# Optimization experiments

Measured on AMD Instinct MI355X. Metric: run time of the kernel, lower is better.

The kernel has to match this reference:

```python
import jax, jax.numpy as jnp
import numpy as np

E = 1024   # embed_dim
H = 16     # num_heads
D = E // H # head_dim = 64
B = 2
S = 2048

def setup_inputs() -> dict:
    key = jax.random.key(0)
    ks = jax.random.split(key, 11)
    std = 0.02
    return {
        "query": jax.random.normal(ks[0], (B, S, E), jnp.float32),
        "key":   jax.random.normal(ks[1], (B, S, E), jnp.float32),
        "value": jax.random.normal(ks[2], (B, S, E), jnp.float32),
        "Wq": std * jax.random.normal(ks[3], (E, E), jnp.float32),
        "bq": jnp.zeros((E,), jnp.float32),
        "Wk": std * jax.random.normal(ks[4], (D, E), jnp.float32),
        "bk": jnp.zeros((D,), jnp.float32),
        "Wv": std * jax.random.normal(ks[5], (D, E), jnp.float32),
        "bv": jnp.zeros((D,), jnp.float32),
        "Wo": std * jax.random.normal(ks[6], (E, E), jnp.float32),
        "bo": jnp.zeros((E,), jnp.float32),
    }

def reference(query, key, value, Wq, bq, Wk, bk, Wv, bv, Wo, bo):
    b, t, _ = query.shape
    scaling = D ** -0.5
    q = query @ Wq.T + bq                      # [B, T, E]
    k = key @ Wk.T + bk                        # [B, S, D] (single shared KV head)
    v = value @ Wv.T + bv                      # [B, S, D]
    q = q.reshape(b, t, H, D).transpose(0, 2, 1, 3) * scaling  # [B, H, T, D]
    # MQA: broadcast shared k/v across heads inside einsum (no materialized expand)
    attn_weights = jnp.einsum("bhtd,bsd->bhts", q, k)          # [B, H, T, S]
    attn_probs = jax.nn.softmax(attn_weights, axis=-1)
    attn_output = jnp.einsum("bhts,bsd->bhtd", attn_probs, v)  # [B, H, T, D]
    attn_output = attn_output.transpose(0, 2, 1, 3).reshape(b, t, E)
    return attn_output @ Wo.T + bo
```

## Files before the change

kernel.cpp:

```cpp
#include <hip/hip_runtime.h>

#define E_DIM  1024
#define H_HEADS 16
#define D_HEAD  64
#define B_BATCH 2
#define S_SEQ  2048
#define M_ROWS (B_BATCH * S_SEQ)

typedef unsigned short u16;
typedef unsigned int   u32;
typedef __attribute__((ext_vector_type(8))) short bf16x8;
typedef __attribute__((ext_vector_type(4))) short bf16x4;
typedef __attribute__((ext_vector_type(4))) float f32x4;

#define MFMA32(a, b, c) __builtin_amdgcn_mfma_f32_16x16x32_bf16(a, b, c, 0, 0, 0)

#if __has_builtin(__builtin_amdgcn_mfma_f32_16x16x16bf16_1k)
#define HAVE_MFMA16 1
#define MFMA16(a, b, c) __builtin_amdgcn_mfma_f32_16x16x16bf16_1k(a, b, c, 0, 0, 0)
#else
#define HAVE_MFMA16 0
#endif

__device__ __forceinline__ u16 f2bf(float f) {
    union { float f; u32 i; } x; x.f = f;
    u32 r = x.i + 0x7fffu + ((x.i >> 16) & 1u);
    return (u16)(r >> 16);
}

#if __has_builtin(__builtin_amdgcn_cvt_pk_bf16_f32)
typedef __attribute__((ext_vector_type(2))) __bf16 bfp2;
__device__ __forceinline__ u32 pk2(float a, float b) {
    bfp2 t = __builtin_amdgcn_cvt_pk_bf16_f32(a, b);
    union { bfp2 v; u32 u; } c; c.v = t; return c.u;
}
#else
__device__ __forceinline__ u32 pk2(float a, float b) {
    return (u32)f2bf(a) | ((u32)f2bf(b) << 16);
}
#endif

__device__ __forceinline__ bf16x8 cvt8(const float4& a, const float4& b) {
    union { u32 u[4]; bf16x8 v; } t;
    t.u[0] = pk2(a.x, a.y); t.u[1] = pk2(a.z, a.w);
    t.u[2] = pk2(b.x, b.y); t.u[3] = pk2(b.z, b.w);
    return t.v;
}
__device__ __forceinline__ bf16x4 pack4(const f32x4& v) {
    union { u32 u[2]; bf16x4 w; } t;
    t.u[0] = pk2(v[0], v[1]); t.u[1] = pk2(v[2], v[3]);
    return t.w;
}

__device__ __forceinline__ void gl_lds16(const u16* g, u16* l) {
    __builtin_amdgcn_global_load_lds(
        (const __attribute__((address_space(1))) u32*)g,
        (__attribute__((address_space(3))) u32*)l, 16, 0, 0);
}

__global__ __launch_bounds__(256) void cast_all_kernel(
    const float* __restrict__ q,  const float* __restrict__ wq,
    const float* __restrict__ wo,
    u16* __restrict__ qo, u16* __restrict__ wqo, u16* __restrict__ woo)
{
    const int bid = blockIdx.x;
    const float* src; u16* dst; size_t base;
    if (bid < 2048)      { src = q;  dst = qo;  base = (size_t)bid * 2048; }
    else if (bid < 2560) { src = wq; dst = wqo; base = (size_t)(bid - 2048) * 2048; }
    else                 { src = wo; dst = woo; base = (size_t)(bid - 2560) * 2048; }
    const size_t i = base + (size_t)threadIdx.x * 8;
    float4 a = ((const float4*)(src + i))[0];
    float4 b = ((const float4*)(src + i))[1];
    *(bf16x8*)(dst + i) = cvt8(a, b);
}

template<bool OUT_BF16>
__global__ __launch_bounds__(256, 2) void gemm_bf16_kernel(
    const u16* __restrict__ A, const u16* __restrict__ W,
    const float* __restrict__ bias, void* __restrict__ Cv,
    int M, int N, int K, float scale)
{
    __shared__ u16 Asm[2][2][128 * 32];
    __shared__ u16 Bsm[2][2][64 * 32];

    const int tid = threadIdx.x;
    const int w  = tid >> 6;
    const int ln = tid & 63;
    const int n  = ln & 15;
    const int qd = ln >> 4;
    const int wm = (w & 1) * 64;
    const int wn = (w >> 1) * 32;

    const int m0 = blockIdx.y * 128;
    const int n0 = blockIdx.x * 64;

    const int srow = tid >> 2;
    const int sblk = tid & 3;
    const int sc   = (sblk ^ (srow & 3)) * 8;

    f32x4 acc[4][2];
#pragma unroll
    for (int mt = 0; mt < 4; mt++)
#pragma unroll
        for (int nt = 0; nt < 2; nt++) acc[mt][nt] = (f32x4){0.f, 0.f, 0.f, 0.f};

    auto stageA = [&](int p, int k0) {
#pragma unroll
        for (int kb = 0; kb < 2; kb++)
#pragma unroll
            for (int g = 0; g < 2; g++) {
                const int row = g * 64 + srow;
                gl_lds16(A + (size_t)(m0 + row) * K + k0 + kb * 32 + sc,
                         &Asm[p][kb][row * 32 + sblk * 8]);
            }
    };
    auto stageB = [&](int p, int k0) {
#pragma unroll
        for (int kb = 0; kb < 2; kb++)
            gl_lds16(W + (size_t)(n0 + srow) * K + k0 + kb * 32 + sc,
                     &Bsm[p][kb][srow * 32 + sblk * 8]);
    };
    auto compute = [&](int p) {
        bf16x8 af[4][2], bfr[2][2];
#pragma unroll
        for (int kb = 0; kb < 2; kb++) {
#pragma unroll
            for (int mt = 0; mt < 4; mt++) {
                const int r = wm + mt * 16 + n;
                af[mt][kb] = *(const bf16x8*)&Asm[p][kb][r * 32 + ((qd ^ (n & 3)) * 8)];
            }
#pragma unroll
            for (int nt = 0; nt < 2; nt++) {
                const int r = wn + nt * 16 + n;
                bfr[nt][kb] = *(const bf16x8*)&Bsm[p][kb][r * 32 + ((qd ^ (n & 3)) * 8)];
            }
        }
#pragma unroll
        for (int kb = 0; kb < 2; kb++)
#pragma unroll
            for (int mt = 0; mt < 4; mt++)
#pragma unroll
                for (int nt = 0; nt < 2; nt++)
                    acc[mt][nt] = MFMA32(af[mt][kb], bfr[nt][kb], acc[mt][nt]);
    };

    stageA(0, 0); stageB(0, 0);

    int p = 0;
    for (int k0 = 64; k0 < K; k0 += 64) {
        __syncthreads();
        stageA(p ^ 1, k0);
        stageB(p ^ 1, k0);
        compute(p);
        p ^= 1;
    }
    __syncthreads();
    compute(p);

    float bb[2];
#pragma unroll
    for (int nt = 0; nt < 2; nt++) bb[nt] = bias[n0 + wn + nt * 16 + n] * scale;

#pragma unroll
    for (int mt = 0; mt < 4; mt++)
#pragma unroll
        for (int r = 0; r < 4; r++) {
            const int row = m0 + wm + mt * 16 + qd * 4 + r;
#pragma unroll
            for (int nt = 0; nt < 2; nt++) {
                const int col = n0 + wn + nt * 16 + n;
                float v = acc[mt][nt][r] * scale + bb[nt];
                if (OUT_BF16) ((u16*)Cv)[(size_t)row * N + col] = f2bf(v);
                else        ((float*)Cv)[(size_t)row * N + col] = v;
            }
        }
}

__global__ __launch_bounds__(256) void kv_proj_kernel(
    const float* __restrict__ key, const float* __restrict__ value,
    const float* __restrict__ Wk, const float* __restrict__ Wv,
    const float* __restrict__ bk, const float* __restrict__ bv,
    u16* __restrict__ Kout, u16* __restrict__ VTout, int M, int K)
{
    const bool vproj = (blockIdx.y == 1);
    const float* A    = vproj ? value : key;
    const float* W    = vproj ? Wv : Wk;
    const float* bias = vproj ? bv : bk;

    __shared__ u16 Asm[64 * 32];
    __shared__ u16 Bsm[64 * 32];

    const int tid = threadIdx.x;
    const int w  = tid >> 6;
    const int ln = tid & 63;
    const int n  = ln & 15;
    const int qd = ln >> 4;
    const int wm = (w & 1) * 32;
    const int wn = (w >> 1) * 32;
    const int m0 = blockIdx.x * 64;

    const int srow = tid >> 2;
    const int scol = (tid & 3) * 8;

    f32x4 acc[2][2];
#pragma unroll
    for (int mt = 0; mt < 2; mt++)
#pragma unroll
        for (int nt = 0; nt < 2; nt++) acc[mt][nt] = (f32x4){0.f, 0.f, 0.f, 0.f};

    for (int k0 = 0; k0 < K; k0 += 32) {
        __syncthreads();
        const float* pa = A + (size_t)(m0 + srow) * K + k0 + scol;
        const float* pw = W + (size_t)srow * K + k0 + scol;
        float4 a0 = ((const float4*)pa)[0], a1 = ((const float4*)pa)[1];
        float4 w0 = ((const float4*)pw)[0], w1 = ((const float4*)pw)[1];
        *(bf16x8*)&Asm[srow * 32 + scol] = cvt8(a0, a1);
        *(bf16x8*)&Bsm[srow * 32 + scol] = cvt8(w0, w1);
        __syncthreads();

        bf16x8 af[2], bfr[2];
#pragma unroll
        for (int t = 0; t < 2; t++) {
            af[t]  = *(const bf16x8*)&Asm[(wm + t * 16 + n) * 32 + qd * 8];
            bfr[t] = *(const bf16x8*)&Bsm[(wn + t * 16 + n) * 32 + qd * 8];
        }
#pragma unroll
        for (int mt = 0; mt < 2; mt++)
#pragma unroll
            for (int nt = 0; nt < 2; nt++)
                acc[mt][nt] = MFMA32(af[mt], bfr[nt], acc[mt][nt]);
    }

    if (!vproj) {
#pragma unroll
        for (int mt = 0; mt < 2; mt++)
#pragma unroll
            for (int r = 0; r < 4; r++) {
                const int row = m0 + wm + mt * 16 + qd * 4 + r;
#pragma unroll
                for (int nt = 0; nt < 2; nt++) {
                    const int col = wn + nt * 16 + n;
                    Kout[(size_t)row * 64 + col] = f2bf(acc[mt][nt][r] + bias[col]);
                }
            }
    } else {
#pragma unroll
        for (int mt = 0; mt < 2; mt++)
#pragma unroll
            for (int nt = 0; nt < 2; nt++) {
                const int col = wn + nt * 16 + n;
                const int row0 = m0 + wm + mt * 16 + qd * 4;
                float b4 = bias[col];
                ushort4 pk;
                pk.x = f2bf(acc[mt][nt][0] + b4);
                pk.y = f2bf(acc[mt][nt][1] + b4);
                pk.z = f2bf(acc[mt][nt][2] + b4);
                pk.w = f2bf(acc[mt][nt][3] + b4);
                *(ushort4*)&VTout[(size_t)col * M + row0] = pk;
            }
    }
}

__global__ __launch_bounds__(256, 3) void mqa_attn_mfma_kernel(
    const u16* Q, const u16* __restrict__ K,
    const u16* __restrict__ VT, u16* O)
{
    __shared__ u16 ksm[2][128 * 32];
    __shared__ u16 vsm[4][64 * 32];
#if !HAVE_MFMA16
    __shared__ u16 psm[4][32 * 128];
#endif

    const int tid = threadIdx.x;
    const int w   = tid >> 6;
    const int ln  = tid & 63;
    const int n   = ln & 15;
    const int qd  = ln >> 4;
    const int lr  = ln >> 2;
    const int blk = ln & 3;
    const int rb  = lr & 3;

    const int bid = blockIdx.x;
    const int qb = bid & 15;
    const int h  = (bid >> 4) & (H_HEADS - 1);
    const int b  = bid >> 8;
    const int q0 = qb * 128;

    {
        const u16* qg = Q + (size_t)(b * S_SEQ + q0) * E_DIM + h * 64;
#pragma unroll
        for (int kb = 0; kb < 2; kb++)
#pragma unroll
            for (int j = 0; j < 2; j++) {
                int row = w * 32 + j * 16 + lr;
                gl_lds16(qg + (size_t)row * E_DIM + kb * 32 + ((blk ^ rb) * 8),
                         &ksm[kb][row * 32 + blk * 8]);
            }
    }
    __syncthreads();

    bf16x8 qa[2][2];
#pragma unroll
    for (int mt = 0; mt < 2; mt++)
#pragma unroll
        for (int kb = 0; kb < 2; kb++) {
            int row = w * 32 + mt * 16 + n;
            qa[mt][kb] = *(const bf16x8*)&ksm[kb][row * 32 + ((qd ^ (n & 3)) * 8)];
        }

    f32x4 acc_o[2][4];
    float lsum[2] = {0.f, 0.f};
#pragma unroll
    for (int mt = 0; mt < 2; mt++)
#pragma unroll
        for (int ntd = 0; ntd < 4; ntd++) acc_o[mt][ntd] = (f32x4){0.f, 0.f, 0.f, 0.f};

    const u16* kg = K  + (size_t)b * S_SEQ * 64;
    const u16* vg = VT + (size_t)b * S_SEQ;

    for (int s0 = 0; s0 < S_SEQ; s0 += 128) {
        __syncthreads();
#pragma unroll
        for (int kb = 0; kb < 2; kb++)
#pragma unroll
            for (int j = 0; j < 2; j++) {
                int row = w * 32 + j * 16 + lr;
                gl_lds16(kg + (size_t)(s0 + row) * 64 + kb * 32 + ((blk ^ rb) * 8),
                         &ksm[kb][row * 32 + blk * 8]);
            }
#pragma unroll
        for (int j = 0; j < 4; j++) {
            int d = j * 16 + lr;
            gl_lds16(vg + (size_t)d * M_ROWS + s0 + w * 32 + ((blk ^ rb) * 8),
                     &vsm[w][d * 32 + blk * 8]);
        }
        __syncthreads();

        f32x4 sacc[2][8];
#pragma unroll
        for (int mt = 0; mt < 2; mt++)
#pragma unroll
            for (int nt = 0; nt < 8; nt++) sacc[mt][nt] = (f32x4){0.f, 0.f, 0.f, 0.f};
#pragma unroll
        for (int nt = 0; nt < 8; nt++) {
            int rowk = nt * 16 + n;
#pragma unroll
            for (int kb = 0; kb < 2; kb++) {
                bf16x8 kf = *(const bf16x8*)&ksm[kb][rowk * 32 + ((qd ^ (n & 3)) * 8)];
                sacc[0][nt] = MFMA32(kf, qa[0][kb], sacc[0][nt]);
                sacc[1][nt] = MFMA32(kf, qa[1][kb], sacc[1][nt]);
            }
        }

        bf16x4 pa[2][8];
#pragma unroll
        for (int mt = 0; mt < 2; mt++) {
            float ls = 0.f;
#pragma unroll
            for (int nt = 0; nt < 8; nt++) {
#pragma unroll
                for (int r = 0; r < 4; r++) {
                    float pv = exp2f(sacc[mt][nt][r]);
                    sacc[mt][nt][r] = pv;
                    ls += pv;
                }
                pa[mt][nt] = pack4(sacc[mt][nt]);
            }
            lsum[mt] += ls;
        }

#if HAVE_MFMA16
#pragma unroll
        for (int kk = 0; kk < 8; kk++) {
            int c = kk >> 1;
            int lblk = (kk & 1) * 2 + (qd >> 1);
#pragma unroll
            for (int ntd = 0; ntd < 4; ntd++) {
                int d = ntd * 16 + n;
                bf16x4 bv = *(const bf16x4*)
                    &vsm[c][d * 32 + ((lblk ^ (n & 3)) * 8) + (qd & 1) * 4];
                acc_o[0][ntd] = MFMA16(pa[0][kk], bv, acc_o[0][ntd]);
                acc_o[1][ntd] = MFMA16(pa[1][kk], bv, acc_o[1][ntd]);
            }
        }
#else
#pragma unroll
        for (int mt = 0; mt < 2; mt++)
#pragma unroll
            for (int nt = 0; nt < 8; nt++) {
                int t = mt * 16 + n;
                int lb = nt * 2 + (qd >> 1);
                union { bf16x4 v; uint2 u; } pw; pw.v = pa[mt][nt];
                *(uint2*)&psm[w][t * 128 + ((lb ^ n) * 8) + (qd & 1) * 4] = pw.u;
            }
#pragma unroll
        for (int kb = 0; kb < 4; kb++) {
            bf16x8 paf[2];
#pragma unroll
            for (int mt = 0; mt < 2; mt++) {
                int t = mt * 16 + n;
                paf[mt] = *(const bf16x8*)&psm[w][t * 128 + (((kb * 4 + qd) ^ n) * 8)];
            }
#pragma unroll
            for (int ntd = 0; ntd < 4; ntd++) {
                int d = ntd * 16 + n;
                bf16x8 bv = *(const bf16x8*)&vsm[kb][d * 32 + ((qd ^ (n & 3)) * 8)];
                acc_o[0][ntd] = MFMA32(paf[0], bv, acc_o[0][ntd]);
                acc_o[1][ntd] = MFMA32(paf[1], bv, acc_o[1][ntd]);
            }
        }
#endif
    }

#pragma unroll
    for (int mt = 0; mt < 2; mt++) {
        lsum[mt] += __shfl_xor(lsum[mt], 16);
        lsum[mt] += __shfl_xor(lsum[mt], 32);
    }
#pragma unroll
    for (int mt = 0; mt < 2; mt++)
#pragma unroll
        for (int r = 0; r < 4; r++) {
            float inv = 1.f / __shfl(lsum[mt], qd * 4 + r);
            int grow = b * S_SEQ + q0 + w * 32 + mt * 16 + qd * 4 + r;
#pragma unroll
            for (int ntd = 0; ntd < 4; ntd++) {
                int gcol = h * D_HEAD + ntd * 16 + n;
                O[(size_t)grow * E_DIM + gcol] = f2bf(acc_o[mt][ntd][r] * inv);
            }
        }
}

extern "C" void kernel_launch(void* const* d_in, const int* in_sizes, int n_in,
                              void* d_out, int out_size, void* d_ws, size_t ws_size,
                              hipStream_t stream) {
    const float* query = (const float*)d_in[0];
    const float* key   = (const float*)d_in[1];
    const float* value = (const float*)d_in[2];
    const float* Wq    = (const float*)d_in[3];
    const float* bq    = (const float*)d_in[4];
    const float* Wk    = (const float*)d_in[5];
    const float* bk    = (const float*)d_in[6];
    const float* Wv    = (const float*)d_in[7];
    const float* bv    = (const float*)d_in[8];
    const float* Wo    = (const float*)d_in[9];
    const float* bo    = (const float*)d_in[10];
    float* out = (float*)d_out;

    const int M = M_ROWS;

    u16* q_bf  = (u16*)d_ws;
    u16* k_bf  = q_bf + (size_t)M * E_DIM;
    u16* vt_bf = k_bf + (size_t)M * D_HEAD;
    u16* wq_bf = vt_bf + (size_t)M * D_HEAD;
    u16* wo_bf = wq_bf + (size_t)E_DIM * E_DIM;

    u16* qc_bf = (u16*)d_out;

    dim3 blk(256);
    const float scaling = 0.125f * 1.44269504088896f;

    cast_all_kernel<<<dim3(3072), blk, 0, stream>>>(
        query, Wq, Wo, qc_bf, wq_bf, wo_bf);

    kv_proj_kernel<<<dim3(M / 64, 2), blk, 0, stream>>>(
        key, value, Wk, Wv, bk, bv, k_bf, vt_bf, M, E_DIM);

    gemm_bf16_kernel<true><<<dim3(E_DIM / 64, M / 128), blk, 0, stream>>>(
        qc_bf, wq_bf, bq, q_bf, M, E_DIM, E_DIM, scaling);

    mqa_attn_mfma_kernel<<<dim3(B_BATCH * H_HEADS * (S_SEQ / 128)), blk, 0, stream>>>(
        q_bf, k_bf, vt_bf, q_bf);

    gemm_bf16_kernel<false><<<dim3(E_DIM / 64, M / 128), blk, 0, stream>>>(
        q_bf, wo_bf, bo, out, M, E_DIM, E_DIM, 1.0f);
}
```

Baseline: 260.6 us.

## Halve attention query tile to 64 rows and raise occupancy

Reduces each attention block's query tile from 128 to 64 rows, giving each wave 16 query rows and doubling the grid size. Register pressure drops, so launch bounds allow 4 blocks per CU. This aims at better occupancy and CU fill. The cost is that each K/V tile is loaded twice as often and each K fragment feeds only one MFMA, which cuts data reuse.

```diff
diff --git a/kernel.cpp b/kernel.cpp
--- a/kernel.cpp
+++ b/kernel.cpp
@@ -261,14 +261,14 @@
     }
 }
 
-__global__ __launch_bounds__(256, 3) void mqa_attn_mfma_kernel(
+__global__ __launch_bounds__(256, 4) void mqa_attn_mfma_kernel(
     const u16* Q, const u16* __restrict__ K,
     const u16* __restrict__ VT, u16* O)
 {
     __shared__ u16 ksm[2][128 * 32];
     __shared__ u16 vsm[4][64 * 32];
 #if !HAVE_MFMA16
-    __shared__ u16 psm[4][32 * 128];
+    __shared__ u16 psm[4][16 * 128];
 #endif
 
     const int tid = threadIdx.x;
@@ -281,39 +281,33 @@
     const int rb  = lr & 3;
 
     const int bid = blockIdx.x;
-    const int qb = bid & 15;
-    const int h  = (bid >> 4) & (H_HEADS - 1);
-    const int b  = bid >> 8;
-    const int q0 = qb * 128;
+    const int qb = bid & 31;
+    const int h  = (bid >> 5) & (H_HEADS - 1);
+    const int b  = bid >> 9;
+    const int q0 = qb * 64;
 
     {
         const u16* qg = Q + (size_t)(b * S_SEQ + q0) * E_DIM + h * 64;
 #pragma unroll
-        for (int kb = 0; kb < 2; kb++)
-#pragma unroll
-            for (int j = 0; j < 2; j++) {
-                int row = w * 32 + j * 16 + lr;
-                gl_lds16(qg + (size_t)row * E_DIM + kb * 32 + ((blk ^ rb) * 8),
-                         &ksm[kb][row * 32 + blk * 8]);
-            }
+        for (int kb = 0; kb < 2; kb++) {
+            int row = w * 16 + lr;
+            gl_lds16(qg + (size_t)row * E_DIM + kb * 32 + ((blk ^ rb) * 8),
+                     &ksm[kb][row * 32 + blk * 8]);
+        }
     }
     __syncthreads();
 
-    bf16x8 qa[2][2];
-#pragma unroll
-    for (int mt = 0; mt < 2; mt++)
-#pragma unroll
-        for (int kb = 0; kb < 2; kb++) {
-            int row = w * 32 + mt * 16 + n;
-            qa[mt][kb] = *(const bf16x8*)&ksm[kb][row * 32 + ((qd ^ (n & 3)) * 8)];
-        }
-
-    f32x4 acc_o[2][4];
-    float lsum[2] = {0.f, 0.f};
-#pragma unroll
-    for (int mt = 0; mt < 2; mt++)
-#pragma unroll
-        for (int ntd = 0; ntd < 4; ntd++) acc_o[mt][ntd] = (f32x4){0.f, 0.f, 0.f, 0.f};
+    bf16x8 qa[2];
+#pragma unroll
+    for (int kb = 0; kb < 2; kb++) {
+        int row = w * 16 + n;
+        qa[kb] = *(const bf16x8*)&ksm[kb][row * 32 + ((qd ^ (n & 3)) * 8)];
+    }
+
+    f32x4 acc_o[4];
+    float lsum = 0.f;
+#pragma unroll
+    for (int ntd = 0; ntd < 4; ntd++) acc_o[ntd] = (f32x4){0.f, 0.f, 0.f, 0.f};
 
     const u16* kg = K  + (size_t)b * S_SEQ * 64;
     const u16* vg = VT + (size_t)b * S_SEQ;
@@ -336,37 +330,33 @@
         }
         __syncthreads();
 
-        f32x4 sacc[2][8];
-#pragma unroll
-        for (int mt = 0; mt < 2; mt++)
-#pragma unroll
-            for (int nt = 0; nt < 8; nt++) sacc[mt][nt] = (f32x4){0.f, 0.f, 0.f, 0.f};
+        f32x4 sacc[8];
+#pragma unroll
+        for (int nt = 0; nt < 8; nt++) sacc[nt] = (f32x4){0.f, 0.f, 0.f, 0.f};
 #pragma unroll
         for (int nt = 0; nt < 8; nt++) {
             int rowk = nt * 16 + n;
 #pragma unroll
             for (int kb = 0; kb < 2; kb++) {
                 bf16x8 kf = *(const bf16x8*)&ksm[kb][rowk * 32 + ((qd ^ (n & 3)) * 8)];
-                sacc[0][nt] = MFMA32(kf, qa[0][kb], sacc[0][nt]);
-                sacc[1][nt] = MFMA32(kf, qa[1][kb], sacc[1][nt]);
-            }
-        }
-
-        bf16x4 pa[2][8];
-#pragma unroll
-        for (int mt = 0; mt < 2; mt++) {
+                sacc[nt] = MFMA32(kf, qa[kb], sacc[nt]);
+            }
+        }
+
+        bf16x4 pa[8];
+        {
             float ls = 0.f;
 #pragma unroll
             for (int nt = 0; nt < 8; nt++) {
 #pragma unroll
                 for (int r = 0; r < 4; r++) {
-                    float pv = exp2f(sacc[mt][nt][r]);
-                    sacc[mt][nt][r] = pv;
+                    float pv = exp2f(sacc[nt][r]);
+                    sacc[nt][r] = pv;
                     ls += pv;
                 }
-                pa[mt][nt] = pack4(sacc[mt][nt]);
-            }
-            lsum[mt] += ls;
+                pa[nt] = pack4(sacc[nt]);
+            }
+            lsum += ls;
         }
 
 #if HAVE_MFMA16
@@ -379,56 +369,43 @@
                 int d = ntd * 16 + n;
                 bf16x4 bv = *(const bf16x4*)
                     &vsm[c][d * 32 + ((lblk ^ (n & 3)) * 8) + (qd & 1) * 4];
-                acc_o[0][ntd] = MFMA16(pa[0][kk], bv, acc_o[0][ntd]);
-                acc_o[1][ntd] = MFMA16(pa[1][kk], bv, acc_o[1][ntd]);
+                acc_o[ntd] = MFMA16(pa[kk], bv, acc_o[ntd]);
             }
         }
 #else
 #pragma unroll
-        for (int mt = 0; mt < 2; mt++)
-#pragma unroll
-            for (int nt = 0; nt < 8; nt++) {
-                int t = mt * 16 + n;
-                int lb = nt * 2 + (qd >> 1);
-                union { bf16x4 v; uint2 u; } pw; pw.v = pa[mt][nt];
-                *(uint2*)&psm[w][t * 128 + ((lb ^ n) * 8) + (qd & 1) * 4] = pw.u;
-            }
+        for (int nt = 0; nt < 8; nt++) {
+            int t = n;
+            int lb = nt * 2 + (qd >> 1);
+            union { bf16x4 v; uint2 u; } pw; pw.v = pa[nt];
+            *(uint2*)&psm[w][t * 128 + ((lb ^ n) * 8) + (qd & 1) * 4] = pw.u;
+        }
 #pragma unroll
         for (int kb = 0; kb < 4; kb++) {
-            bf16x8 paf[2];
-#pragma unroll
-            for (int mt = 0; mt < 2; mt++) {
-                int t = mt * 16 + n;
-                paf[mt] = *(const bf16x8*)&psm[w][t * 128 + (((kb * 4 + qd) ^ n) * 8)];
-            }
+            int t = n;
+            bf16x8 paf = *(const bf16x8*)&psm[w][t * 128 + (((kb * 4 + qd) ^ n) * 8)];
 #pragma unroll
             for (int ntd = 0; ntd < 4; ntd++) {
                 int d = ntd * 16 + n;
                 bf16x8 bv = *(const bf16x8*)&vsm[kb][d * 32 + ((qd ^ (n & 3)) * 8)];
-                acc_o[0][ntd] = MFMA32(paf[0], bv, acc_o[0][ntd]);
-                acc_o[1][ntd] = MFMA32(paf[1], bv, acc_o[1][ntd]);
+                acc_o[ntd] = MFMA32(paf, bv, acc_o[ntd]);
             }
         }
 #endif
     }
 
-#pragma unroll
-    for (int mt = 0; mt < 2; mt++) {
-        lsum[mt] += __shfl_xor(lsum[mt], 16);
-        lsum[mt] += __shfl_xor(lsum[mt], 32);
-    }
-#pragma unroll
-    for (int mt = 0; mt < 2; mt++)
-#pragma unroll
-        for (int r = 0; r < 4; r++) {
-            float inv = 1.f / __shfl(lsum[mt], qd * 4 + r);
-            int grow = b * S_SEQ + q0 + w * 32 + mt * 16 + qd * 4 + r;
-#pragma unroll
-            for (int ntd = 0; ntd < 4; ntd++) {
-                int gcol = h * D_HEAD + ntd * 16 + n;
-                O[(size_t)grow * E_DIM + gcol] = f2bf(acc_o[mt][ntd][r] * inv);
-            }
-        }
+    lsum += __shfl_xor(lsum, 16);
+    lsum += __shfl_xor(lsum, 32);
+#pragma unroll
+    for (int r = 0; r < 4; r++) {
+        float inv = 1.f / __shfl(lsum, qd * 4 + r);
+        int grow = b * S_SEQ + q0 + w * 16 + qd * 4 + r;
+#pragma unroll
+        for (int ntd = 0; ntd < 4; ntd++) {
+            int gcol = h * D_HEAD + ntd * 16 + n;
+            O[(size_t)grow * E_DIM + gcol] = f2bf(acc_o[ntd][r] * inv);
+        }
+    }
 }
 
 extern "C" void kernel_launch(void* const* d_in, const int* in_sizes, int n_in,
@@ -469,7 +446,7 @@
     gemm_bf16_kernel<true><<<dim3(E_DIM / 64, M / 128), blk, 0, stream>>>(
         qc_bf, wq_bf, bq, q_bf, M, E_DIM, E_DIM, scaling);
 
-    mqa_attn_mfma_kernel<<<dim3(B_BATCH * H_HEADS * (S_SEQ / 128)), blk, 0, stream>>>(
+    mqa_attn_mfma_kernel<<<dim3(B_BATCH * H_HEADS * (S_SEQ / 64)), blk, 0, stream>>>(
         q_bf, k_bf, vt_bf, q_bf);
 
     gemm_bf16_kernel<false><<<dim3(E_DIM / 64, M / 128), blk, 0, stream>>>(
```

Measured after the change: 272.2 us. 1.04x slower.

## Merge cast and KV projection into one prep kernel; widen LDS XOR swizzle

Applied to the files above, without the earlier changes.

The separate cast and KV-projection kernels become one prep_kernel. The first 128 blocks do the K/V projections and the rest do the bf16 casts, which saves a launch and lets the two kinds of work overlap. The LDS swizzle in the GEMM and attention kernels now also XORs in higher row bits ((n&3)^(n>>2)), so 16-byte fragment reads from rows that previously mapped to the same banks are spread across more banks. Mixing heavy projection blocks with light cast blocks in one grid could cause scheduling imbalance.

```diff
diff --git a/kernel.cpp b/kernel.cpp
--- a/kernel.cpp
+++ b/kernel.cpp
@@ -58,146 +58,46 @@
         (__attribute__((address_space(3))) u32*)l, 16, 0, 0);
 }
 
-__global__ __launch_bounds__(256) void cast_all_kernel(
-    const float* __restrict__ q,  const float* __restrict__ wq,
-    const float* __restrict__ wo,
-    u16* __restrict__ qo, u16* __restrict__ wqo, u16* __restrict__ woo)
-{
-    const int bid = blockIdx.x;
-    const float* src; u16* dst; size_t base;
-    if (bid < 2048)      { src = q;  dst = qo;  base = (size_t)bid * 2048; }
-    else if (bid < 2560) { src = wq; dst = wqo; base = (size_t)(bid - 2048) * 2048; }
-    else                 { src = wo; dst = woo; base = (size_t)(bid - 2560) * 2048; }
-    const size_t i = base + (size_t)threadIdx.x * 8;
-    float4 a = ((const float4*)(src + i))[0];
-    float4 b = ((const float4*)(src + i))[1];
-    *(bf16x8*)(dst + i) = cvt8(a, b);
-}
-
-template<bool OUT_BF16>
-__global__ __launch_bounds__(256, 2) void gemm_bf16_kernel(
-    const u16* __restrict__ A, const u16* __restrict__ W,
-    const float* __restrict__ bias, void* __restrict__ Cv,
-    int M, int N, int K, float scale)
-{
-    __shared__ u16 Asm[2][2][128 * 32];
-    __shared__ u16 Bsm[2][2][64 * 32];
-
-    const int tid = threadIdx.x;
-    const int w  = tid >> 6;
-    const int ln = tid & 63;
-    const int n  = ln & 15;
-    const int qd = ln >> 4;
-    const int wm = (w & 1) * 64;
-    const int wn = (w >> 1) * 32;
-
-    const int m0 = blockIdx.y * 128;
-    const int n0 = blockIdx.x * 64;
-
-    const int srow = tid >> 2;
-    const int sblk = tid & 3;
-    const int sc   = (sblk ^ (srow & 3)) * 8;
-
-    f32x4 acc[4][2];
-#pragma unroll
-    for (int mt = 0; mt < 4; mt++)
-#pragma unroll
-        for (int nt = 0; nt < 2; nt++) acc[mt][nt] = (f32x4){0.f, 0.f, 0.f, 0.f};
-
-    auto stageA = [&](int p, int k0) {
-#pragma unroll
-        for (int kb = 0; kb < 2; kb++)
-#pragma unroll
-            for (int g = 0; g < 2; g++) {
-                const int row = g * 64 + srow;
-                gl_lds16(A + (size_t)(m0 + row) * K + k0 + kb * 32 + sc,
-                         &Asm[p][kb][row * 32 + sblk * 8]);
-            }
-    };
-    auto stageB = [&](int p, int k0) {
-#pragma unroll
-        for (int kb = 0; kb < 2; kb++)
-            gl_lds16(W + (size_t)(n0 + srow) * K + k0 + kb * 32 + sc,
-                     &Bsm[p][kb][srow * 32 + sblk * 8]);
-    };
-    auto compute = [&](int p) {
-        bf16x8 af[4][2], bfr[2][2];
-#pragma unroll
-        for (int kb = 0; kb < 2; kb++) {
-#pragma unroll
-            for (int mt = 0; mt < 4; mt++) {
-                const int r = wm + mt * 16 + n;
-                af[mt][kb] = *(const bf16x8*)&Asm[p][kb][r * 32 + ((qd ^ (n & 3)) * 8)];
-            }
-#pragma unroll
-            for (int nt = 0; nt < 2; nt++) {
-                const int r = wn + nt * 16 + n;
-                bfr[nt][kb] = *(const bf16x8*)&Bsm[p][kb][r * 32 + ((qd ^ (n & 3)) * 8)];
-            }
-        }
-#pragma unroll
-        for (int kb = 0; kb < 2; kb++)
-#pragma unroll
-            for (int mt = 0; mt < 4; mt++)
-#pragma unroll
-                for (int nt = 0; nt < 2; nt++)
-                    acc[mt][nt] = MFMA32(af[mt][kb], bfr[nt][kb], acc[mt][nt]);
-    };
-
-    stageA(0, 0); stageB(0, 0);
-
-    int p = 0;
-    for (int k0 = 64; k0 < K; k0 += 64) {
-        __syncthreads();
-        stageA(p ^ 1, k0);
-        stageB(p ^ 1, k0);
-        compute(p);
-        p ^= 1;
-    }
-    __syncthreads();
-    compute(p);
-
-    float bb[2];
-#pragma unroll
-    for (int nt = 0; nt < 2; nt++) bb[nt] = bias[n0 + wn + nt * 16 + n] * scale;
-
-#pragma unroll
-    for (int mt = 0; mt < 4; mt++)
-#pragma unroll
-        for (int r = 0; r < 4; r++) {
-            const int row = m0 + wm + mt * 16 + qd * 4 + r;
-#pragma unroll
-            for (int nt = 0; nt < 2; nt++) {
-                const int col = n0 + wn + nt * 16 + n;
-                float v = acc[mt][nt][r] * scale + bb[nt];
-                if (OUT_BF16) ((u16*)Cv)[(size_t)row * N + col] = f2bf(v);
-                else        ((float*)Cv)[(size_t)row * N + col] = v;
-            }
-        }
-}
-
-__global__ __launch_bounds__(256) void kv_proj_kernel(
+__global__ __launch_bounds__(256) void prep_kernel(
+    const float* __restrict__ query, const float* __restrict__ Wq,
+    const float* __restrict__ Wo,
+    u16* __restrict__ qc, u16* __restrict__ wq_bf, u16* __restrict__ wo_bf,
     const float* __restrict__ key, const float* __restrict__ value,
     const float* __restrict__ Wk, const float* __restrict__ Wv,
     const float* __restrict__ bk, const float* __restrict__ bv,
     u16* __restrict__ Kout, u16* __restrict__ VTout, int M, int K)
 {
-    const bool vproj = (blockIdx.y == 1);
+    __shared__ u16 Asm[64 * 32];
+    __shared__ u16 Bsm[64 * 32];
+
+    const int bid = blockIdx.x;
+    const int tid = threadIdx.x;
+
+    if (bid >= 128) {
+        const int cbid = bid - 128;
+        const float* src; u16* dst; size_t base;
+        if (cbid < 2048)      { src = query; dst = qc;    base = (size_t)cbid * 2048; }
+        else if (cbid < 2560) { src = Wq;    dst = wq_bf; base = (size_t)(cbid - 2048) * 2048; }
+        else                  { src = Wo;    dst = wo_bf; base = (size_t)(cbid - 2560) * 2048; }
+        const size_t i = base + (size_t)tid * 8;
+        float4 a = ((const float4*)(src + i))[0];
+        float4 b = ((const float4*)(src + i))[1];
+        *(bf16x8*)(dst + i) = cvt8(a, b);
+        return;
+    }
+
+    const bool vproj = (bid >= 64);
     const float* A    = vproj ? value : key;
     const float* W    = vproj ? Wv : Wk;
     const float* bias = vproj ? bv : bk;
 
-    __shared__ u16 Asm[64 * 32];
-    __shared__ u16 Bsm[64 * 32];
-
-    const int tid = threadIdx.x;
     const int w  = tid >> 6;
     const int ln = tid & 63;
     const int n  = ln & 15;
     const int qd = ln >> 4;
     const int wm = (w & 1) * 32;
     const int wn = (w >> 1) * 32;
-    const int m0 = blockIdx.x * 64;
+    const int m0 = (bid & 63) * 64;
 
     const int srow = tid >> 2;
     const int scol = (tid & 3) * 8;
@@ -261,6 +161,109 @@
     }
 }
 
+template<bool OUT_BF16>
+__global__ __launch_bounds__(256, 2) void gemm_bf16_kernel(
+    const u16* __restrict__ A, const u16* __restrict__ W,
+    const float* __restrict__ bias, void* __restrict__ Cv,
+    int M, int N, int K, float scale)
+{
+    __shared__ u16 Asm[2][2][128 * 32];
+    __shared__ u16 Bsm[2][2][64 * 32];
+
+    const int tid = threadIdx.x;
+    const int w  = tid >> 6;
+    const int ln = tid & 63;
+    const int n  = ln & 15;
+    const int qd = ln >> 4;
+    const int ns = (n & 3) ^ (n >> 2);
+    const int wm = (w & 1) * 64;
+    const int wn = (w >> 1) * 32;
+
+    const int m0 = blockIdx.y * 128;
+    const int n0 = blockIdx.x * 64;
+
+    const int srow = tid >> 2;
+    const int sblk = tid & 3;
+    const int sc   = ((sblk ^ (srow & 3) ^ ((srow >> 2) & 3)) * 8);
+
+    f32x4 acc[4][2];
+#pragma unroll
+    for (int mt = 0; mt < 4; mt++)
+#pragma unroll
+        for (int nt = 0; nt < 2; nt++) acc[mt][nt] = (f32x4){0.f, 0.f, 0.f, 0.f};
+
+    auto stageA = [&](int p, int k0) {
+#pragma unroll
+        for (int kb = 0; kb < 2; kb++)
+#pragma unroll
+            for (int g = 0; g < 2; g++) {
+                const int row = g * 64 + srow;
+                gl_lds16(A + (size_t)(m0 + row) * K + k0 + kb * 32 + sc,
+                         &Asm[p][kb][row * 32 + sblk * 8]);
+            }
+    };
+    auto stageB = [&](int p, int k0) {
+#pragma unroll
+        for (int kb = 0; kb < 2; kb++)
+            gl_lds16(W + (size_t)(n0 + srow) * K + k0 + kb * 32 + sc,
+                     &Bsm[p][kb][srow * 32 + sblk * 8]);
+    };
+    auto compute = [&](int p) {
+        bf16x8 af[4][2], bfr[2][2];
+#pragma unroll
+        for (int kb = 0; kb < 2; kb++) {
+#pragma unroll
+            for (int mt = 0; mt < 4; mt++) {
+                const int r = wm + mt * 16 + n;
+                af[mt][kb] = *(const bf16x8*)&Asm[p][kb][r * 32 + ((qd ^ ns) * 8)];
+            }
+#pragma unroll
+            for (int nt = 0; nt < 2; nt++) {
+                const int r = wn + nt * 16 + n;
+                bfr[nt][kb] = *(const bf16x8*)&Bsm[p][kb][r * 32 + ((qd ^ ns) * 8)];
+            }
+        }
+#pragma unroll
+        for (int kb = 0; kb < 2; kb++)
+#pragma unroll
+            for (int mt = 0; mt < 4; mt++)
+#pragma unroll
+                for (int nt = 0; nt < 2; nt++)
+                    acc[mt][nt] = MFMA32(af[mt][kb], bfr[nt][kb], acc[mt][nt]);
+    };
+
+    stageA(0, 0); stageB(0, 0);
+
+    int p = 0;
+    for (int k0 = 64; k0 < K; k0 += 64) {
+        __syncthreads();
+        stageA(p ^ 1, k0);
+        stageB(p ^ 1, k0);
+        compute(p);
+        p ^= 1;
+    }
+    __syncthreads();
+    compute(p);
+
+    float bb[2];
+#pragma unroll
+    for (int nt = 0; nt < 2; nt++) bb[nt] = bias[n0 + wn + nt * 16 + n] * scale;
+
+#pragma unroll
+    for (int mt = 0; mt < 4; mt++)
+#pragma unroll
+        for (int r = 0; r < 4; r++) {
+            const int row = m0 + wm + mt * 16 + qd * 4 + r;
+#pragma unroll
+            for (int nt = 0; nt < 2; nt++) {
+                const int col = n0 + wn + nt * 16 + n;
+                float v = acc[mt][nt][r] * scale + bb[nt];
+                if (OUT_BF16) ((u16*)Cv)[(size_t)row * N + col] = f2bf(v);
+                else        ((float*)Cv)[(size_t)row * N + col] = v;
+            }
+        }
+}
+
 __global__ __launch_bounds__(256, 3) void mqa_attn_mfma_kernel(
     const u16* Q, const u16* __restrict__ K,
     const u16* __restrict__ VT, u16* O)
@@ -278,7 +281,8 @@
     const int qd  = ln >> 4;
     const int lr  = ln >> 2;
     const int blk = ln & 3;
-    const int rb  = lr & 3;
+    const int ns  = (n & 3) ^ (n >> 2);
+    const int rs  = (lr & 3) ^ (lr >> 2);
 
     const int bid = blockIdx.x;
     const int qb = bid & 15;
@@ -293,7 +297,7 @@
 #pragma unroll
             for (int j = 0; j < 2; j++) {
                 int row = w * 32 + j * 16 + lr;
-                gl_lds16(qg + (size_t)row * E_DIM + kb * 32 + ((blk ^ rb) * 8),
+                gl_lds16(qg + (size_t)row * E_DIM + kb * 32 + ((blk ^ rs) * 8),
                          &ksm[kb][row * 32 + blk * 8]);
             }
     }
@@ -305,7 +309,7 @@
 #pragma unroll
         for (int kb = 0; kb < 2; kb++) {
             int row = w * 32 + mt * 16 + n;
-            qa[mt][kb] = *(const bf16x8*)&ksm[kb][row * 32 + ((qd ^ (n & 3)) * 8)];
+            qa[mt][kb] = *(const bf16x8*)&ksm[kb][row * 32 + ((qd ^ ns) * 8)];
         }
 
     f32x4 acc_o[2][4];
@@ -325,13 +329,13 @@
 #pragma unroll
             for (int j = 0; j < 2; j++) {
                 int row = w * 32 + j * 16 + lr;
-                gl_lds16(kg + (size_t)(s0 + row) * 64 + kb * 32 + ((blk ^ rb) * 8),
+                gl_lds16(kg + (size_t)(s0 + row) * 64 + kb * 32 + ((blk ^ rs) * 8),
                          &ksm[kb][row * 32 + blk * 8]);
             }
 #pragma unroll
         for (int j = 0; j < 4; j++) {
             int d = j * 16 + lr;
-            gl_lds16(vg + (size_t)d * M_ROWS + s0 + w * 32 + ((blk ^ rb) * 8),
+            gl_lds16(vg + (size_t)d * M_ROWS + s0 + w * 32 + ((blk ^ rs) * 8),
                      &vsm[w][d * 32 + blk * 8]);
         }
         __syncthreads();
@@ -346,7 +350,7 @@
             int rowk = nt * 16 + n;
 #pragma unroll
             for (int kb = 0; kb < 2; kb++) {
-                bf16x8 kf = *(const bf16x8*)&ksm[kb][rowk * 32 + ((qd ^ (n & 3)) * 8)];
+                bf16x8 kf = *(const bf16x8*)&ksm[kb][rowk * 32 + ((qd ^ ns) * 8)];
                 sacc[0][nt] = MFMA32(kf, qa[0][kb], sacc[0][nt]);
                 sacc[1][nt] = MFMA32(kf, qa[1][kb], sacc[1][nt]);
             }
@@ -378,7 +382,7 @@
             for (int ntd = 0; ntd < 4; ntd++) {
                 int d = ntd * 16 + n;
                 bf16x4 bv = *(const bf16x4*)
-                    &vsm[c][d * 32 + ((lblk ^ (n & 3)) * 8) + (qd & 1) * 4];
+                    &vsm[c][d * 32 + ((lblk ^ ns) * 8) + (qd & 1) * 4];
                 acc_o[0][ntd] = MFMA16(pa[0][kk], bv, acc_o[0][ntd]);
                 acc_o[1][ntd] = MFMA16(pa[1][kk], bv, acc_o[1][ntd]);
             }
@@ -404,7 +408,7 @@
 #pragma unroll
             for (int ntd = 0; ntd < 4; ntd++) {
                 int d = ntd * 16 + n;
-                bf16x8 bv = *(const bf16x8*)&vsm[kb][d * 32 + ((qd ^ (n & 3)) * 8)];
+                bf16x8 bv = *(const bf16x8*)&vsm[kb][d * 32 + ((qd ^ ns) * 8)];
                 acc_o[0][ntd] = MFMA32(paf[0], bv, acc_o[0][ntd]);
                 acc_o[1][ntd] = MFMA32(paf[1], bv, acc_o[1][ntd]);
             }
@@ -460,10 +464,8 @@
     dim3 blk(256);
     const float scaling = 0.125f * 1.44269504088896f;
 
-    cast_all_kernel<<<dim3(3072), blk, 0, stream>>>(
-        query, Wq, Wo, qc_bf, wq_bf, wo_bf);
-
-    kv_proj_kernel<<<dim3(M / 64, 2), blk, 0, stream>>>(
+    prep_kernel<<<dim3(3200), blk, 0, stream>>>(
+        query, Wq, Wo, qc_bf, wq_bf, wo_bf,
         key, value, Wk, Wv, bk, bv, k_bf, vt_bf, M, E_DIM);
 
     gemm_bf16_kernel<true><<<dim3(E_DIM / 64, M / 128), blk, 0, stream>>>(
```

Result: faster. 251.1 us (-3.7%).
